# Kernel optimization log

Measured on AMD Instinct MI355X. Metric: run time of the kernel, lower is better.

## Reference

```python
import jax, jax.numpy as jnp
import numpy as np

B, T, W_IN = 64, 512, 40
KS = 3
N = KS * KS          # 9 sampling points
CF = 8               # conv filters
GH = 32              # GRU hidden
GIN = (W_IN - KS + 1) * CF  # 304
ATTN = 32


def setup_inputs() -> dict:
    key = jax.random.key(0)
    ks = jax.random.split(key, 10)
    p = {}
    p["x"] = jax.random.normal(ks[0], (B, 1, T, W_IN), jnp.float32)
    p["p_w"] = jax.random.normal(ks[1], (2 * N, 1, KS, KS), jnp.float32) * 0.01
    p["p_b"] = jnp.zeros((2 * N,), jnp.float32)
    p["dcn_w"] = jax.random.normal(ks[2], (CF, 1, KS, KS), jnp.float32) * 0.1
    p["dcn_b"] = jnp.zeros((CF,), jnp.float32)
    p["w_ih"] = jax.random.normal(ks[3], (3 * GH, GIN), jnp.float32) * 0.05
    p["w_hh"] = jax.random.normal(ks[4], (3 * GH, GH), jnp.float32) * 0.05
    p["b_ih"] = jnp.zeros((3 * GH,), jnp.float32)
    p["b_hh"] = jnp.zeros((3 * GH,), jnp.float32)
    p["w1"] = jax.random.normal(ks[5], (ATTN, GH), jnp.float32) * 0.1
    p["b1"] = jnp.zeros((ATTN,), jnp.float32)
    p["w2"] = jax.random.normal(ks[6], (GH, ATTN), jnp.float32) * 0.1
    p["b2"] = jnp.zeros((GH,), jnp.float32)
    p["w3"] = jax.random.normal(ks[7], (2, GH), jnp.float32) * 0.1
    p["b3"] = jnp.zeros((2,), jnp.float32)
    return p


def _deform_conv(x, p_w, p_b, w, b):
    # x: (B,1,H,W). Deform-conv v1: offsets from a VALID 3x3 conv, bilinear gather.
    Bb, C, H, W = x.shape
    offset = jax.lax.conv_general_dilated(
        x, p_w, (1, 1), "VALID",
        dimension_numbers=("NCHW", "OIHW", "NCHW")) + p_b[None, :, None, None]
    h, w_ = offset.shape[2], offset.shape[3]  # (T-2, 38)
    r = KS // 2
    pny, pnx = jnp.meshgrid(jnp.arange(-r, r + 1), jnp.arange(-r, r + 1), indexing="ij")
    p0y, p0x = jnp.meshgrid(jnp.arange(1, h + 1), jnp.arange(1, w_ + 1), indexing="ij")
    py = offset[:, :N] + pny.reshape(1, N, 1, 1) + p0y[None, None]  # (B,N,h,w)
    px = offset[:, N:] + pnx.reshape(1, N, 1, 1) + p0x[None, None]
    py = jnp.clip(py, 0.0, H - 1.0)
    px = jnp.clip(px, 0.0, W - 1.0)
    y0 = jnp.floor(py).astype(jnp.int32)
    x0 = jnp.floor(px).astype(jnp.int32)
    y1 = jnp.minimum(y0 + 1, H - 1)
    x1 = jnp.minimum(x0 + 1, W - 1)
    wy = (py - y0)[:, None]  # (B,1,N,h,w)
    wx = (px - x0)[:, None]
    flat = x.reshape(Bb, C, H * W)

    def gather(yi, xi):
        idx = (yi * W + xi).reshape(Bb, 1, -1)
        g = jnp.take_along_axis(flat, idx, axis=2)
        return g.reshape(Bb, C, N, h, w_)

    g00 = gather(y0, x0); g01 = gather(y0, x1)
    g10 = gather(y1, x0); g11 = gather(y1, x1)
    samp = (g00 * (1 - wy) * (1 - wx) + g01 * (1 - wy) * wx
            + g10 * wy * (1 - wx) + g11 * wy * wx)  # (B,C,N,h,w)
    out = jnp.einsum("bcnhw,ocn->bohw", samp, w.reshape(w.shape[0], C, N))
    return out + b[None, :, None, None]


def _gru(seq, w_ih, w_hh, b_ih, b_hh):
    # seq: (T,B,GIN); PyTorch GRU equations, single layer, h0 = 0
    xp = jnp.einsum("tbi,hi->tbh", seq, w_ih) + b_ih  # (T,B,3H)
    h0 = jnp.zeros((seq.shape[1], GH), seq.dtype)

    def step(hprev, xt):
        hp = hprev @ w_hh.T + b_hh
        xr, xz, xn = jnp.split(xt, 3, axis=-1)
        hr, hz, hn = jnp.split(hp, 3, axis=-1)
        rg = jax.nn.sigmoid(xr + hr)
        zg = jax.nn.sigmoid(xz + hz)
        ng = jnp.tanh(xn + rg * hn)
        hnew = (1 - zg) * ng + zg * hprev
        return hnew, hnew

    _, ys = jax.lax.scan(step, h0, xp)
    return ys  # (T,B,GH)


def _forward(x, p_w, p_b, dcn_w, dcn_b, w_ih, w_hh, b_ih, b_hh, w1, b1, w2, b2, w3, b3):
    y = _deform_conv(x, p_w, p_b, dcn_w, dcn_b)        # (B,CF,h,w)
    h = y.shape[2]
    y = jnp.transpose(y, (2, 0, 3, 1)).reshape(h, y.shape[1], -1)  # wait
    return y


def _model(x, p_w, p_b, dcn_w, dcn_b, w_ih, w_hh, b_ih, b_hh, w1, b1, w2, b2, w3, b3):
    y = _deform_conv(x, p_w, p_b, dcn_w, dcn_b)        # (B,CF,h,w)
    Bb = y.shape[0]
    h = y.shape[2]
    seq = jnp.transpose(y, (2, 0, 3, 1)).reshape(h, Bb, -1)  # (h,B,w*CF) w-major then channel
    enc = jnp.transpose(_gru(seq, w_ih, w_hh, b_ih, b_hh), (1, 0, 2))  # (B,h,GH)
    a = jnp.tanh(enc @ w1.T + b1) @ w2.T + b2          # (B,h,GH)
    a = jax.nn.softmax(a, axis=1)                      # softmax over time
    pooled = jnp.sum(a * enc, axis=1)                  # (B,GH)
    return pooled @ w3.T + b3                          # (B,2)


def reference(x, p_w, p_b, dcn_w, dcn_b, w_ih, w_hh, b_ih, b_hh, w1, b1, w2, b2, w3, b3):
    return _model(x, p_w, p_b, dcn_w, dcn_b, w_ih, w_hh, b_ih, b_hh, w1, b1, w2, b2, w3, b3)
```

## Files before the change

kernel.cpp:

```cpp
#include <hip/hip_runtime.h>
#include <math.h>
#include <stdint.h>

#define BB 64
#define TT 512
#define W_IN 40
#define CF 8
#define GH 32
#define HOUT 510
#define WOUT 38
#define GIN 304
#define G3 96
#define ATT 32
#define MROWS (HOUT * BB)

#define LOG2E 1.4426950408889634f

__device__ __forceinline__ float fast_rcp(float x) {
#if defined(__has_builtin)
# if __has_builtin(__builtin_amdgcn_rcpf)
    return __builtin_amdgcn_rcpf(x);
# else
    return 1.f / x;
# endif
#else
    return 1.f / x;
#endif
}

__device__ __forceinline__ float fast_exp2(float x) {
#if defined(__has_builtin)
# if __has_builtin(__builtin_amdgcn_exp2f)
    return __builtin_amdgcn_exp2f(x);
# else
    return exp2f(x);
# endif
#else
    return exp2f(x);
#endif
}

typedef __attribute__((address_space(3))) uint32_t lds_u32_t;
typedef const __attribute__((address_space(1))) uint32_t glb_u32_t;

#if defined(__has_builtin) && __has_builtin(__builtin_amdgcn_global_load_lds)
#define HAS_GLL 1
#else
#define HAS_GLL 0
#endif

#define KC2 152
#define WI_C 19
__global__ __launch_bounds__(192, 1) void k_dcn_gemm_fused(
    const float* __restrict__ x, const float* __restrict__ p_w, const float* __restrict__ p_b,
    const float* __restrict__ dcn_w, const float* __restrict__ dcn_b,
    const float* __restrict__ w_ih, const float* __restrict__ b_ih,
    float* __restrict__ xp)
{
    __shared__ float As[128 * KC2];
    __shared__ float Ws[96 * KC2];
    __shared__ float pw_s[162], pb_s[18], dw_s[72], db_s[8];

    const int tid = threadIdx.x;
    const int t0  = blockIdx.x * 2;
    const int r0  = blockIdx.x * 128;
    const int mg  = tid / 12;
    const int ng  = tid % 12;

    if (tid < 162) pw_s[tid] = p_w[tid];
    if (tid < 18)  pb_s[tid] = p_b[tid];
    if (tid < 72)  dw_s[tid] = dcn_w[tid];
    if (tid < 8)   db_s[tid] = dcn_b[tid];

    float bih[8];
    #pragma unroll
    for (int j = 0; j < 8; ++j) bih[j] = b_ih[ng + 12 * j];

    float acc[8][8];
    #pragma unroll
    for (int i = 0; i < 8; ++i)
        #pragma unroll
        for (int j = 0; j < 8; ++j) acc[i][j] = 0.f;

    auto stageW = [&](int ch) {
        for (int u4 = tid; u4 < 96 * (KC2 / 4); u4 += 192) {
            const int g   = u4 / (KC2 / 4);
            const int k4l = u4 % (KC2 / 4);
            const float* src = w_ih + (size_t)g * GIN + ch * KC2 + k4l * 4;
            float* dst = &Ws[u4 * 4];
#if HAS_GLL
            __builtin_amdgcn_global_load_lds((glb_u32_t*)(uintptr_t)src,
                                             (lds_u32_t*)(uintptr_t)dst, 16, 0, 0);
#else
            *(float4*)dst = *(const float4*)src;
#endif
        }
    };

    auto phaseA = [&](int ch) {
        for (int item = tid; item < 128 * WI_C; item += 192) {
            const int lr = item / WI_C;
            const int wl = item % WI_C;
            const int wi = ch * WI_C + wl;
            const int t  = t0 + (lr >> 6);
            const int b  = lr & 63;
            const float* xb = x + (size_t)b * TT * W_IN;

            float patch[9];
            #pragma unroll
            for (int ky = 0; ky < 3; ++ky)
                #pragma unroll
                for (int kx = 0; kx < 3; ++kx)
                    patch[ky * 3 + kx] = xb[(t + ky) * W_IN + wi + kx];

            float offs[18];
            #pragma unroll
            for (int n = 0; n < 18; ++n) {
                float a = pb_s[n];
                #pragma unroll
                for (int k = 0; k < 9; ++k) a += patch[k] * pw_s[n * 9 + k];
                offs[n] = a;
            }

            float samp[9];
            #pragma unroll
            for (int n = 0; n < 9; ++n) {
                float py = offs[n]     + (float)(n / 3 - 1) + (float)(t + 1);
                float px = offs[9 + n] + (float)(n % 3 - 1) + (float)(wi + 1);
                py = fminf(fmaxf(py, 0.f), (float)(TT - 1));
                px = fminf(fmaxf(px, 0.f), (float)(W_IN - 1));
                float fy = floorf(py), fx = floorf(px);
                int y0 = (int)fy, x0 = (int)fx;
                int y1 = min(y0 + 1, TT - 1), x1 = min(x0 + 1, W_IN - 1);
                float wy = py - fy, wx = px - fx;
                float g00 = xb[y0 * W_IN + x0], g01 = xb[y0 * W_IN + x1];
                float g10 = xb[y1 * W_IN + x0], g11 = xb[y1 * W_IN + x1];
                samp[n] = g00 * (1.f - wy) * (1.f - wx) + g01 * (1.f - wy) * wx
                        + g10 * wy * (1.f - wx) + g11 * wy * wx;
            }

            float o[CF];
            #pragma unroll
            for (int c = 0; c < CF; ++c) {
                float a = db_s[c];
                #pragma unroll
                for (int n = 0; n < 9; ++n) a += samp[n] * dw_s[c * 9 + n];
                o[c] = a;
            }
            float* arow = &As[lr * KC2 + wl * 8];
            ((float4*)arow)[0] = make_float4(o[0], o[1], o[2], o[3]);
            ((float4*)arow)[1] = make_float4(o[4], o[5], o[6], o[7]);
        }
    };

    auto gemm = [&]() {
        #pragma unroll 2
        for (int k4 = 0; k4 < KC2 / 4; ++k4) {
            float4 a[8], w[8];
            #pragma unroll
            for (int i = 0; i < 8; ++i)
                a[i] = *(const float4*)&As[(mg + 16 * i) * KC2 + k4 * 4];
            #pragma unroll
            for (int j = 0; j < 8; ++j)
                w[j] = *(const float4*)&Ws[(ng + 12 * j) * KC2 + k4 * 4];
            #pragma unroll
            for (int i = 0; i < 8; ++i)
                #pragma unroll
                for (int j = 0; j < 8; ++j)
                    acc[i][j] += a[i].x * w[j].x + a[i].y * w[j].y
                               + a[i].z * w[j].z + a[i].w * w[j].w;
        }
    };

    __syncthreads();
    stageW(0);
    phaseA(0);
    __syncthreads();
    gemm();
    __syncthreads();
    stageW(1);
    phaseA(1);
    __syncthreads();
    gemm();

    #pragma unroll
    for (int i = 0; i < 8; ++i) {
        const int row = r0 + mg + 16 * i;
        #pragma unroll
        for (int j = 0; j < 8; ++j)
            xp[(size_t)row * G3 + ng + 12 * j] = acc[i][j] + bih[j];
    }
}

#define GCH 16
#define NCH 32

__global__ __launch_bounds__(64) void k_gru(
    const float* __restrict__ xp, const float* __restrict__ w_hh,
    const float* __restrict__ b_hh, float* __restrict__ enc)
{
    __shared__ float xs[2][GCH * G3];

    const int l = threadIdx.x;
    const int half = l >> 5;
    const int j = l & 31;
    const int b = blockIdx.x;

    float wr[16], wz[16], wn[16];
    #pragma unroll
    for (int i = 0; i < 16; ++i) {
        wr[i] = w_hh[(size_t)j * GH + half * 16 + i];
        wz[i] = w_hh[(size_t)(GH + j) * GH + half * 16 + i];
        wn[i] = w_hh[(size_t)(2 * GH + j) * GH + half * 16 + i];
    }
    const float br = b_hh[j], bz = b_hh[GH + j], bn = b_hh[2 * GH + j];

    auto stage = [&](int c, int buf) {
        #pragma unroll
        for (int k = 0; k < 6; ++k) {
            const int f  = k * 256 + l * 4;
            const int tl = f / 96;
            const int g  = f % 96;
            int gt = c * GCH + tl;
            if (gt > HOUT - 1) gt = HOUT - 1;
            const float* src = xp + ((size_t)gt * BB + b) * G3 + g;
            float* dst = &xs[buf][k * 256];
#if HAS_GLL
            __builtin_amdgcn_global_load_lds((glb_u32_t*)(uintptr_t)src,
                                             (lds_u32_t*)(uintptr_t)dst, 16, 0, 0);
#else
            *(float4*)(&xs[buf][f]) = *(const float4*)src;
#endif
        }
    };

    stage(0, 0);
    float h = 0.f;

    #pragma unroll 1
    for (int c = 0; c < NCH; ++c) {
        const int buf = c & 1;
        if (c + 1 < NCH) {
            stage(c + 1, buf ^ 1);
            asm volatile("s_waitcnt vmcnt(6)" ::: "memory");
        } else {
            asm volatile("s_waitcnt vmcnt(0)" ::: "memory");
        }
        const int nst = (c == NCH - 1) ? (HOUT - (NCH - 1) * GCH) : GCH;
        #pragma unroll 1
        for (int tl = 0; tl < nst; ++tl) {
            const float* xrow = &xs[buf][tl * G3];
            const float xr = xrow[j], xz = xrow[GH + j], xn = xrow[2 * GH + j];

            float pr0 = 0.f, pr1 = 0.f, pr2 = 0.f, pr3 = 0.f;
            float pz0 = 0.f, pz1 = 0.f, pz2 = 0.f, pz3 = 0.f;
            float pn0 = 0.f, pn1 = 0.f, pn2 = 0.f, pn3 = 0.f;
            #pragma unroll
            for (int i = 0; i < 16; i += 4) {
                const float h0 = __shfl(h, half * 16 + i + 0, 64);
                const float h1 = __shfl(h, half * 16 + i + 1, 64);
                const float h2 = __shfl(h, half * 16 + i + 2, 64);
                const float h3 = __shfl(h, half * 16 + i + 3, 64);
                pr0 += wr[i + 0] * h0; pr1 += wr[i + 1] * h1;
                pr2 += wr[i + 2] * h2; pr3 += wr[i + 3] * h3;
                pz0 += wz[i + 0] * h0; pz1 += wz[i + 1] * h1;
                pz2 += wz[i + 2] * h2; pz3 += wz[i + 3] * h3;
                pn0 += wn[i + 0] * h0; pn1 += wn[i + 1] * h1;
                pn2 += wn[i + 2] * h2; pn3 += wn[i + 3] * h3;
            }
            const float pr = (pr0 + pr1) + (pr2 + pr3);
            const float pz = (pz0 + pz1) + (pz2 + pz3);
            const float pn = (pn0 + pn1) + (pn2 + pn3);
            const float ar = br + pr + __shfl_xor(pr, 32, 64);
            const float az = bz + pz + __shfl_xor(pz, 32, 64);
            const float an = bn + pn + __shfl_xor(pn, 32, 64);

            const float rg = fast_rcp(1.f + fast_exp2(-(xr + ar) * LOG2E));
            const float zg = fast_rcp(1.f + fast_exp2(-(xz + az) * LOG2E));
            const float pre = xn + rg * an;
            const float e2 = fast_exp2(pre * (2.f * LOG2E));
            const float tg = 1.f - 2.f * fast_rcp(e2 + 1.f);
            h = (1.f - zg) * tg + zg * h;

            const int t = c * GCH + tl;
            if (!half) enc[((size_t)b * HOUT + t) * GH + j] = h;
        }
    }
}

__global__ __launch_bounds__(256) void k_attn_part(
    const float* __restrict__ enc,
    const float* __restrict__ w1, const float* __restrict__ b1,
    const float* __restrict__ w2, const float* __restrict__ b2,
    float* __restrict__ part)
{
    __shared__ float w1s[ATT * 33], w2s[GH * 33];
    __shared__ float b1s[ATT], b2s[GH];
    __shared__ float encs[8][GH], apres[8][ATT];
    __shared__ float rm[8 * GH], rs[8 * GH], rp[8 * GH];

    const int b   = blockIdx.x >> 2;
    const int c   = blockIdx.x & 3;
    const int tid = threadIdx.x;
    const int ttl = tid >> 5;
    const int j   = tid & 31;

    for (int i = tid; i < ATT * GH; i += 256) {
        int r = i >> 5, cc = i & 31;
        w1s[r * 33 + cc] = w1[i];
        w2s[r * 33 + cc] = w2[i];
    }
    if (tid < ATT)           b1s[tid] = b1[tid];
    else if (tid < ATT + GH) b2s[tid - ATT] = b2[tid - ATT];
    __syncthreads();

    const int tbeg = c * 128;
    const int tend = min(HOUT, tbeg + 128);

    float m = -INFINITY, s = 0.f, p = 0.f;
    const float* encb = enc + (size_t)b * HOUT * GH;

    for (int t0 = tbeg; t0 < tend; t0 += 8) {
        const int t = t0 + ttl;
        const bool act = (t < tend);
        const float ev = act ? encb[t * GH + j] : 0.f;
        encs[ttl][j] = ev;
        __syncthreads();

        float a1 = b1s[j];
        #pragma unroll
        for (int k = 0; k < GH; ++k) a1 += encs[ttl][k] * w1s[j * 33 + k];
        apres[ttl][j] = tanhf(a1);
        __syncthreads();

        float a2 = b2s[j];
        #pragma unroll
        for (int k = 0; k < ATT; ++k) a2 += apres[ttl][k] * w2s[j * 33 + k];

        if (act) {
            float mn = fmaxf(m, a2);
            float sc = expf(m - mn);
            float e  = expf(a2 - mn);
            s = s * sc + e;
            p = p * sc + e * ev;
            m = mn;
        }
        __syncthreads();
    }

    rm[tid] = m; rs[tid] = s; rp[tid] = p;
    __syncthreads();

    if (tid < GH) {
        float M = -INFINITY;
        #pragma unroll
        for (int q = 0; q < 8; ++q) M = fmaxf(M, rm[q * GH + tid]);
        float S = 0.f, P = 0.f;
        #pragma unroll
        for (int q = 0; q < 8; ++q) {
            float sc = expf(rm[q * GH + tid] - M);
            S += rs[q * GH + tid] * sc;
            P += rp[q * GH + tid] * sc;
        }
        float* pb = part + ((size_t)b * 4 + c) * 96;
        pb[tid] = M; pb[32 + tid] = S; pb[64 + tid] = P;
    }
}

__global__ __launch_bounds__(64) void k_attn_fin(
    const float* __restrict__ part,
    const float* __restrict__ w3, const float* __restrict__ b3,
    float* __restrict__ out)
{
    __shared__ float pooled[GH];
    const int b = blockIdx.x;
    const int tid = threadIdx.x;

    if (tid < GH) {
        const float* pb = part + (size_t)b * 4 * 96;
        float M = -INFINITY;
        #pragma unroll
        for (int c = 0; c < 4; ++c) M = fmaxf(M, pb[c * 96 + tid]);
        float S = 0.f, P = 0.f;
        #pragma unroll
        for (int c = 0; c < 4; ++c) {
            float sc = expf(pb[c * 96 + tid] - M);
            S += pb[c * 96 + 32 + tid] * sc;
            P += pb[c * 96 + 64 + tid] * sc;
        }
        pooled[tid] = P / S;
    }
    __syncthreads();

    if (tid < 2) {
        float a = b3[tid];
        #pragma unroll
        for (int k = 0; k < GH; ++k) a += pooled[k] * w3[tid * GH + k];
        out[b * 2 + tid] = a;
    }
}

extern "C" void kernel_launch(void* const* d_in, const int* in_sizes, int n_in,
                              void* d_out, int out_size, void* d_ws, size_t ws_size,
                              hipStream_t stream)
{
    const float* x     = (const float*)d_in[0];
    const float* p_w   = (const float*)d_in[1];
    const float* p_b   = (const float*)d_in[2];
    const float* dcn_w = (const float*)d_in[3];
    const float* dcn_b = (const float*)d_in[4];
    const float* w_ih  = (const float*)d_in[5];
    const float* w_hh  = (const float*)d_in[6];
    const float* b_ih  = (const float*)d_in[7];
    const float* b_hh  = (const float*)d_in[8];
    const float* w1    = (const float*)d_in[9];
    const float* b1    = (const float*)d_in[10];
    const float* w2    = (const float*)d_in[11];
    const float* b2    = (const float*)d_in[12];
    const float* w3    = (const float*)d_in[13];
    const float* b3    = (const float*)d_in[14];
    float* out = (float*)d_out;

    const size_t XP_F = (size_t)MROWS * G3;
    float* xp   = (float*)d_ws;
    float* enc  = xp + XP_F;
    float* part = xp;

    hipLaunchKernelGGL(k_dcn_gemm_fused, dim3(MROWS / 128), dim3(192), 0, stream,
                       x, p_w, p_b, dcn_w, dcn_b, w_ih, b_ih, xp);
    hipLaunchKernelGGL(k_gru, dim3(BB), dim3(64), 0, stream,
                       xp, w_hh, b_hh, enc);
    hipLaunchKernelGGL(k_attn_part, dim3(BB * 4), dim3(256), 0, stream,
                       enc, w1, b1, w2, b2, part);
    hipLaunchKernelGGL(k_attn_fin, dim3(BB), dim3(64), 0, stream,
                       part, w3, b3, out);
}
```

Before: 380.4 us.

## Split fused DCN+GEMM across more blocks with smaller per-block tiles

The fused deformable-conv plus input-projection kernel now uses one time step by half the gate outputs per block, giving 1020 blocks of 256 threads instead of 255 blocks of 192. The goal is more parallelism and occupancy across the many CUs, using smaller accumulator tiles and a padded W tile in LDS. The cost is that the deformable conv work is computed twice, once per output half, and the async global_load_lds staging is replaced by plain float4 loads. The overall kernel time may still be dominated by the sequential GRU kernel.

```diff
diff --git a/kernel.cpp b/kernel.cpp
--- a/kernel.cpp
+++ b/kernel.cpp
@@ -49,61 +49,46 @@
 #define HAS_GLL 0
 #endif
 
-#define KC2 152
+#define KCH 152
+#define WSP 156
 #define WI_C 19
-__global__ __launch_bounds__(192, 1) void k_dcn_gemm_fused(
+
+__global__ __launch_bounds__(256, 2) void k_dcn_gemm2(
     const float* __restrict__ x, const float* __restrict__ p_w, const float* __restrict__ p_b,
     const float* __restrict__ dcn_w, const float* __restrict__ dcn_b,
     const float* __restrict__ w_ih, const float* __restrict__ b_ih,
     float* __restrict__ xp)
 {
-    __shared__ float As[128 * KC2];
-    __shared__ float Ws[96 * KC2];
+    __shared__ float As[64 * KCH];
+    __shared__ float Ws[48 * WSP];
     __shared__ float pw_s[162], pb_s[18], dw_s[72], db_s[8];
 
     const int tid = threadIdx.x;
-    const int t0  = blockIdx.x * 2;
-    const int r0  = blockIdx.x * 128;
-    const int mg  = tid / 12;
-    const int ng  = tid % 12;
+    const int t   = blockIdx.x >> 1;
+    const int n0  = (blockIdx.x & 1) * 48;
+    const int mg  = tid >> 4;
+    const int ng  = tid & 15;
 
     if (tid < 162) pw_s[tid] = p_w[tid];
     if (tid < 18)  pb_s[tid] = p_b[tid];
     if (tid < 72)  dw_s[tid] = dcn_w[tid];
     if (tid < 8)   db_s[tid] = dcn_b[tid];
 
-    float bih[8];
+    float bih[3];
     #pragma unroll
-    for (int j = 0; j < 8; ++j) bih[j] = b_ih[ng + 12 * j];
-
-    float acc[8][8];
+    for (int j = 0; j < 3; ++j) bih[j] = b_ih[n0 + ng + 16 * j];
+
+    float acc[4][3];
     #pragma unroll
-    for (int i = 0; i < 8; ++i)
-        #pragma unroll
-        for (int j = 0; j < 8; ++j) acc[i][j] = 0.f;
-
-    auto stageW = [&](int ch) {
-        for (int u4 = tid; u4 < 96 * (KC2 / 4); u4 += 192) {
-            const int g   = u4 / (KC2 / 4);
-            const int k4l = u4 % (KC2 / 4);
-            const float* src = w_ih + (size_t)g * GIN + ch * KC2 + k4l * 4;
-            float* dst = &Ws[u4 * 4];
-#if HAS_GLL
-            __builtin_amdgcn_global_load_lds((glb_u32_t*)(uintptr_t)src,
-                                             (lds_u32_t*)(uintptr_t)dst, 16, 0, 0);
-#else
-            *(float4*)dst = *(const float4*)src;
-#endif
-        }
-    };
+    for (int i = 0; i < 4; ++i)
+        #pragma unroll
+        for (int j = 0; j < 3; ++j) acc[i][j] = 0.f;
 
     auto phaseA = [&](int ch) {
-        for (int item = tid; item < 128 * WI_C; item += 192) {
-            const int lr = item / WI_C;
+        for (int item = tid; item < 64 * WI_C; item += 256) {
+            const int b  = item / WI_C;
             const int wl = item % WI_C;
             const int wi = ch * WI_C + wl;
-            const int t  = t0 + (lr >> 6);
-            const int b  = lr & 63;
             const float* xb = x + (size_t)b * TT * W_IN;
 
             float patch[9];
@@ -147,48 +132,61 @@
                 for (int n = 0; n < 9; ++n) a += samp[n] * dw_s[c * 9 + n];
                 o[c] = a;
             }
-            float* arow = &As[lr * KC2 + wl * 8];
+            float* arow = &As[b * KCH + wl * 8];
             ((float4*)arow)[0] = make_float4(o[0], o[1], o[2], o[3]);
             ((float4*)arow)[1] = make_float4(o[4], o[5], o[6], o[7]);
         }
     };
 
+    auto stageW = [&](int ch) {
+        #pragma unroll
+        for (int p = 0; p < 8; ++p) {
+            const int u4 = tid + p * 256;
+            if (u4 < 48 * (KCH / 4)) {
+                const int row = u4 / (KCH / 4);
+                const int k4  = u4 % (KCH / 4);
+                float4 v = *(const float4*)(w_ih + (size_t)(n0 + row) * GIN
+                                            + ch * KCH + k4 * 4);
+                *(float4*)(&Ws[row * WSP + k4 * 4]) = v;
+            }
+        }
+    };
+
     auto gemm = [&]() {
         #pragma unroll 2
-        for (int k4 = 0; k4 < KC2 / 4; ++k4) {
-            float4 a[8], w[8];
-            #pragma unroll
-            for (int i = 0; i < 8; ++i)
-                a[i] = *(const float4*)&As[(mg + 16 * i) * KC2 + k4 * 4];
-            #pragma unroll
-            for (int j = 0; j < 8; ++j)
-                w[j] = *(const float4*)&Ws[(ng + 12 * j) * KC2 + k4 * 4];
-            #pragma unroll
-            for (int i = 0; i < 8; ++i)
+        for (int k4 = 0; k4 < KCH / 4; ++k4) {
+            float4 a[4], w[3];
+            #pragma unroll
+            for (int i = 0; i < 4; ++i)
+                a[i] = *(const float4*)&As[(mg + 16 * i) * KCH + k4 * 4];
+            #pragma unroll
+            for (int j = 0; j < 3; ++j)
+                w[j] = *(const float4*)&Ws[(ng + 16 * j) * WSP + k4 * 4];
+            #pragma unroll
+            for (int i = 0; i < 4; ++i)
                 #pragma unroll
-                for (int j = 0; j < 8; ++j)
+                for (int j = 0; j < 3; ++j)
                     acc[i][j] += a[i].x * w[j].x + a[i].y * w[j].y
                                + a[i].z * w[j].z + a[i].w * w[j].w;
         }
     };
 
     __syncthreads();
-    stageW(0);
-    phaseA(0);
-    __syncthreads();
-    gemm();
-    __syncthreads();
-    stageW(1);
-    phaseA(1);
-    __syncthreads();
-    gemm();
+    #pragma unroll 1
+    for (int ch = 0; ch < 2; ++ch) {
+        phaseA(ch);
+        stageW(ch);
+        __syncthreads();
+        gemm();
+        __syncthreads();
+    }
 
     #pragma unroll
-    for (int i = 0; i < 8; ++i) {
-        const int row = r0 + mg + 16 * i;
-        #pragma unroll
-        for (int j = 0; j < 8; ++j)
-            xp[(size_t)row * G3 + ng + 12 * j] = acc[i][j] + bih[j];
+    for (int i = 0; i < 4; ++i) {
+        const int row = t * BB + mg + 16 * i;
+        #pragma unroll
+        for (int j = 0; j < 3; ++j)
+            xp[(size_t)row * G3 + n0 + ng + 16 * j] = acc[i][j] + bih[j];
     }
 }
 
@@ -426,7 +424,7 @@
     float* enc  = xp + XP_F;
     float* part = xp;
 
-    hipLaunchKernelGGL(k_dcn_gemm_fused, dim3(MROWS / 128), dim3(192), 0, stream,
+    hipLaunchKernelGGL(k_dcn_gemm2, dim3(HOUT * 2), dim3(256), 0, stream,
                        x, p_w, p_b, dcn_w, dcn_b, w_ih, b_ih, xp);
     hipLaunchKernelGGL(k_gru, dim3(BB), dim3(64), 0, stream,
                        xp, w_hh, b_hh, enc);
```

Result: slower. 593.1 us (+55.9%).
